# Kernel tuning notes

Hardware: AMD Instinct MI355X
Metric: run time of the kernel (lower is better)

The kernel has to match this reference:

```python
import jax, jax.numpy as jnp
import numpy as np

C = 256; HEADS = 8; LEVELS = 4; POINTS = 4; D = C // HEADS
SPATIAL = np.array([[96, 96], [48, 48], [24, 24], [12, 12]], dtype=np.int32)  # (H, W) per level
AREAS = SPATIAL[:, 0] * SPATIAL[:, 1]
HW = int(AREAS.sum())  # 12240
LSI = np.concatenate([[0], np.cumsum(AREAS)[:-1]]).astype(np.int32)
N = 1; Q = HW


def setup_inputs() -> dict:
    key = jax.random.key(0)
    ks = jax.random.split(key, 12)
    s = 0.02
    return {
        "query": jax.random.normal(ks[0], (N, Q, C), jnp.float32),
        "reference_points": jax.random.uniform(ks[1], (N, Q, LEVELS, 2), jnp.float32),
        "input_flatten": jax.random.normal(ks[2], (N, HW, C), jnp.float32),
        "input_spatial_shapes": jnp.asarray(SPATIAL),
        "input_level_start_index": jnp.asarray(LSI),
        "W_off": jax.random.normal(ks[3], (C, HEADS * LEVELS * POINTS * 2), jnp.float32) * s,
        "b_off": jax.random.normal(ks[4], (HEADS * LEVELS * POINTS * 2,), jnp.float32) * s,
        "W_attn": jax.random.normal(ks[5], (C, HEADS * LEVELS * POINTS), jnp.float32) * s,
        "b_attn": jax.random.normal(ks[6], (HEADS * LEVELS * POINTS,), jnp.float32) * s,
        "W_val": jax.random.normal(ks[7], (C, C), jnp.float32) * (1.0 / np.sqrt(C)),
        "b_val": jax.random.normal(ks[8], (C,), jnp.float32) * s,
        "W_out": jax.random.normal(ks[9], (C, C), jnp.float32) * (1.0 / np.sqrt(C)),
        "b_out": jax.random.normal(ks[10], (C,), jnp.float32) * s,
    }


def _ms_deform_attn(query, reference_points, input_flatten, sp, lsi,
                    W_off, b_off, W_attn, b_attn, W_val, b_val, W_out, b_out):
    n, q, c = query.shape
    hw = input_flatten.shape[1]
    # value projection -> [N, Hd, HW, D]
    value = (input_flatten @ W_val + b_val).reshape(n, hw, HEADS, D).transpose(0, 2, 1, 3)
    # sampling offsets [N,Q,Hd,L,P,2]
    off = (query @ W_off + b_off).reshape(n, q, HEADS, LEVELS, POINTS, 2)
    # attention weights softmaxed over L*P (done inside the fused CUDA kernel)
    attn = jax.nn.softmax((query @ W_attn + b_attn).reshape(n, q, HEADS, LEVELS * POINTS), axis=-1)
    attn = attn.reshape(n, q, HEADS, LEVELS, POINTS)
    # normalized sampling locations (reference_points last dim == 2 branch)
    norm = jnp.stack([sp[:, 1], sp[:, 0]], -1).astype(query.dtype)  # (W, H) per level
    loc = reference_points[:, :, None, :, None, :] + off / norm[None, None, None, :, None, :]
    Hl = sp[:, 0][None, None, None, :, None]
    Wl = sp[:, 1][None, None, None, :, None]
    start = lsi[None, None, None, :, None]
    # grid_sample-style (align_corners=False) pixel coordinates
    x = loc[..., 0] * Wl - 0.5
    y = loc[..., 1] * Hl - 0.5
    x0 = jnp.floor(x); y0 = jnp.floor(y)
    lx = x - x0; ly = y - y0
    x0i = x0.astype(jnp.int32); y0i = y0.astype(jnp.int32)

    def gather(yi, xi):
        valid = (xi >= 0) & (xi < Wl) & (yi >= 0) & (yi < Hl)
        idx = jnp.where(valid, start + yi * Wl + xi, 0)  # [N,Q,Hd,L,P]
        idx_t = idx.transpose(0, 2, 1, 3, 4).reshape(n, HEADS, q * LEVELS * POINTS, 1)
        g = jnp.take_along_axis(value, idx_t, axis=2)  # [N,Hd,Q*L*P,D]
        g = g.reshape(n, HEADS, q, LEVELS, POINTS, D)
        return g * valid.transpose(0, 2, 1, 3, 4)[..., None]

    def w(a):
        return a.transpose(0, 2, 1, 3, 4)[..., None]  # [N,Hd,Q,L,P,1]

    sampled = (gather(y0i, x0i) * w((1 - ly) * (1 - lx))
               + gather(y0i, x0i + 1) * w((1 - ly) * lx)
               + gather(y0i + 1, x0i) * w(ly * (1 - lx))
               + gather(y0i + 1, x0i + 1) * w(ly * lx))  # [N,Hd,Q,L,P,D]
    out = jnp.einsum('nhqlpd,nqhlp->nqhd', sampled, attn).reshape(n, q, c)
    return out @ W_out + b_out


def reference(query, reference_points, input_flatten, input_spatial_shapes, input_level_start_index,
              W_off, b_off, W_attn, b_attn, W_val, b_val, W_out, b_out):
    return _ms_deform_attn(query, reference_points, input_flatten,
                           input_spatial_shapes, input_level_start_index,
                           W_off, b_off, W_attn, b_attn, W_val, b_val, W_out, b_out)
```

## Files before the change

kernel.cpp:

```cpp
#include <hip/hip_runtime.h>

#define QTOT   12240
#define HWTOT  12240
#define KDIM   256

typedef float f32x4 __attribute__((ext_vector_type(4)));
typedef short s16x8 __attribute__((ext_vector_type(8)));
typedef unsigned short ushort_t;

__device__ __forceinline__ unsigned short f2b(float x) {
    union { float f; unsigned u; } c; c.f = x;
    unsigned r = c.u + 0x7fffu + ((c.u >> 16) & 1u);
    return (unsigned short)(r >> 16);
}

#define AEL 783360
__global__ __launch_bounds__(256) void conv_kernel(
    const float* __restrict__ inflat, const float* __restrict__ query,
    const float* __restrict__ W_val, const float* __restrict__ W_off,
    const float* __restrict__ W_attn, const float* __restrict__ W_out,
    const float* __restrict__ b_off, const float* __restrict__ b_attn,
    ushort_t* __restrict__ inflat_b, ushort_t* __restrict__ query_b,
    ushort_t* __restrict__ WvT, ushort_t* __restrict__ WcT,
    ushort_t* __restrict__ WoT, float* __restrict__ bcomb)
{
    int id = blockIdx.x * 256 + threadIdx.x;
    if (id < 2 * AEL) {
        const float* src = (id < AEL) ? inflat : query;
        ushort_t* dst = (id < AEL) ? inflat_b : query_b;
        int t = (id < AEL) ? id : id - AEL;
        float4 f = ((const float4*)src)[t];
        ushort4 o;
        o.x = f2b(f.x); o.y = f2b(f.y); o.z = f2b(f.z); o.w = f2b(f.w);
        ((ushort4*)dst)[t] = o;
    } else if (id < 2 * AEL + 65536) {
        int t = id - 2 * AEL;
        int n = t >> 8, k = t & 255;
        WvT[t] = f2b(W_val[k * 256 + n]);
    } else if (id < 2 * AEL + 65536 + 98304) {
        int t = id - (2 * AEL + 65536);
        int n = t >> 8, k = t & 255;
        float v = (n < 256) ? W_off[k * 256 + n] : W_attn[k * 128 + (n - 256)];
        WcT[t] = f2b(v);
    } else if (id < 2 * AEL + 65536 + 98304 + 65536) {
        int t = id - (2 * AEL + 65536 + 98304);
        int n = t >> 8, k = t & 255;
        WoT[t] = f2b(W_out[k * 256 + n]);
    } else if (id < 2 * AEL + 229376 + 384) {
        int t = id - (2 * AEL + 229376);
        bcomb[t] = (t < 256) ? b_off[t] : b_attn[t - 256];
    }
}

__device__ __forceinline__ void mm_core(
    const ushort_t* __restrict__ A, const ushort_t* __restrict__ BT,
    int bm, int bn, ushort_t As[64][72], ushort_t Bs[64][72], f32x4 acc[2][2])
{
    const int tid = threadIdx.x, lane = tid & 63, wave = tid >> 6;
    const int wr = wave >> 1, wc = wave & 1;
    const int r = tid >> 2, ks = (tid & 3) * 16;
    const bool aval = (bm + r) < QTOT;
    const int lr = lane & 15, g8 = (lane >> 4) * 8;

    for (int k0 = 0; k0 < KDIM; k0 += 64) {
        s16x8 a0 = (s16x8)0, a1 = (s16x8)0;
        if (aval) {
            const s16x8* s = (const s16x8*)(A + (size_t)(bm + r) * KDIM + k0 + ks);
            a0 = s[0]; a1 = s[1];
        }
        const s16x8* t = (const s16x8*)(BT + (size_t)(bn + r) * KDIM + k0 + ks);
        s16x8 b0 = t[0], b1 = t[1];
        if (k0) __syncthreads();
        *(s16x8*)&As[r][ks]     = a0;
        *(s16x8*)&As[r][ks + 8] = a1;
        *(s16x8*)&Bs[r][ks]     = b0;
        *(s16x8*)&Bs[r][ks + 8] = b1;
        __syncthreads();
#pragma unroll
        for (int kk = 0; kk < 2; ++kk) {
            s16x8 af[2], bf[2];
            af[0] = *(const s16x8*)&As[wr * 32 + lr][kk * 32 + g8];
            af[1] = *(const s16x8*)&As[wr * 32 + 16 + lr][kk * 32 + g8];
            bf[0] = *(const s16x8*)&Bs[wc * 32 + lr][kk * 32 + g8];
            bf[1] = *(const s16x8*)&Bs[wc * 32 + 16 + lr][kk * 32 + g8];
#pragma unroll
            for (int m = 0; m < 2; ++m)
#pragma unroll
                for (int n = 0; n < 2; ++n)
                    acc[m][n] = __builtin_amdgcn_mfma_f32_16x16x32_bf16(
                        af[m], bf[n], acc[m][n], 0, 0, 0);
        }
    }
}

__global__ __launch_bounds__(256) void gemm_vc(
    const ushort_t* __restrict__ Ab, const ushort_t* __restrict__ Qb,
    const ushort_t* __restrict__ WvT, const ushort_t* __restrict__ WcT,
    const float* __restrict__ b_val, const float* __restrict__ bcomb,
    ushort_t* __restrict__ projb, ushort_t* __restrict__ offb,
    float* __restrict__ logitf)
{
    __shared__ ushort_t As[64][72], Bs[64][72];
    const int b = blockIdx.x;
    const bool isval = b < 768;
    const ushort_t* A;
    const ushort_t* BT;
    const float* bias;
    int bm, bn;
    if (isval) { A = Ab; BT = WvT; bias = b_val;  bm = (b >> 2) * 64; bn = (b & 3) * 64; }
    else { int t = b - 768; A = Qb; BT = WcT; bias = bcomb; bm = (t / 6) * 64; bn = (t % 6) * 64; }

    f32x4 acc[2][2];
#pragma unroll
    for (int m = 0; m < 2; ++m)
#pragma unroll
        for (int n = 0; n < 2; ++n) acc[m][n] = (f32x4)0.f;

    mm_core(A, BT, bm, bn, As, Bs, acc);

    const int lane = threadIdx.x & 63, wave = threadIdx.x >> 6;
    const int wr = wave >> 1, wc = wave & 1;
    const int lr = lane & 15, rg = (lane >> 4) * 4;
#pragma unroll
    for (int n = 0; n < 2; ++n) {
        const int col = bn + wc * 32 + n * 16 + lr;
        const float bb = bias[col];
#pragma unroll
        for (int m = 0; m < 2; ++m)
#pragma unroll
            for (int rr = 0; rr < 4; ++rr) {
                const int row = bm + wr * 32 + m * 16 + rg + rr;
                if (row >= QTOT) continue;
                const float v = acc[m][n][rr] + bb;
                if (isval)            projb[(size_t)row * 256 + col] = f2b(v);
                else if (col < 256)   offb [(size_t)row * 256 + col] = f2b(v);
                else                  logitf[(size_t)row * 128 + col - 256] = v;
            }
    }
}

__global__ __launch_bounds__(256) void gemm_o(
    const ushort_t* __restrict__ Ab, const ushort_t* __restrict__ WoT,
    const float* __restrict__ b_out, float* __restrict__ out)
{
    __shared__ ushort_t As[64][72], Bs[64][72];
    const int b = blockIdx.x;
    const int bm = (b >> 2) * 64, bn = (b & 3) * 64;

    f32x4 acc[2][2];
#pragma unroll
    for (int m = 0; m < 2; ++m)
#pragma unroll
        for (int n = 0; n < 2; ++n) acc[m][n] = (f32x4)0.f;

    mm_core(Ab, WoT, bm, bn, As, Bs, acc);

    const int lane = threadIdx.x & 63, wave = threadIdx.x >> 6;
    const int wr = wave >> 1, wc = wave & 1;
    const int lr = lane & 15, rg = (lane >> 4) * 4;
#pragma unroll
    for (int n = 0; n < 2; ++n) {
        const int col = bn + wc * 32 + n * 16 + lr;
        const float bb = b_out[col];
#pragma unroll
        for (int m = 0; m < 2; ++m)
#pragma unroll
            for (int rr = 0; rr < 4; ++rr) {
                const int row = bm + wr * 32 + m * 16 + rg + rr;
                if (row < QTOT) out[(size_t)row * 256 + col] = acc[m][n][rr] + bb;
            }
    }
}

__global__ __launch_bounds__(256) void sample3(
    const float* __restrict__ rp, const ushort_t* __restrict__ offb,
    const float* __restrict__ logitf, const ushort_t* __restrict__ projb,
    const int* __restrict__ sp, const int* __restrict__ lsi,
    ushort_t* __restrict__ outpre)
{
    const int bid = blockIdx.x;
    const int q = (bid & 7) * (QTOT / 8) + (bid >> 3);
    const int tid = threadIdx.x;

    __shared__ int   s_idx[128][4];
    __shared__ float s_w[128][4];

    if (tid < 128) {
        const int l = (tid >> 2) & 3;
        float logit = logitf[(size_t)q * 128 + tid];
        float mx = logit;
#pragma unroll
        for (int d = 1; d < 16; d <<= 1) mx = fmaxf(mx, __shfl_xor(mx, d));
        float e = __expf(logit - mx);
        float s = e;
#pragma unroll
        for (int d = 1; d < 16; d <<= 1) s += __shfl_xor(s, d);
        const float aw = e / s;

        const unsigned opk = *(const unsigned*)&offb[(size_t)q * 256 + tid * 2];
        const float ox = __uint_as_float(opk << 16);
        const float oy = __uint_as_float(opk & 0xffff0000u);

        const int Hl = sp[l * 2], Wl = sp[l * 2 + 1], st = lsi[l];
        const float rx = rp[((size_t)q * 4 + l) * 2 + 0];
        const float ry = rp[((size_t)q * 4 + l) * 2 + 1];

        const float x = rx * (float)Wl + ox - 0.5f;
        const float y = ry * (float)Hl + oy - 0.5f;
        const float xf = floorf(x), yf = floorf(y);
        const int x0 = (int)xf, y0 = (int)yf;
        const float lx = x - xf, ly = y - yf;

        const bool vx0 = (x0 >= 0) && (x0 < Wl);
        const bool vx1 = (x0 + 1 >= 0) && (x0 + 1 < Wl);
        const bool vy0 = (y0 >= 0) && (y0 < Hl);
        const bool vy1 = (y0 + 1 >= 0) && (y0 + 1 < Hl);

        s_w[tid][0] = (vx0 && vy0) ? aw * (1.f - ly) * (1.f - lx) : 0.f;
        s_w[tid][1] = (vx1 && vy0) ? aw * (1.f - ly) * lx         : 0.f;
        s_w[tid][2] = (vx0 && vy1) ? aw * ly * (1.f - lx)         : 0.f;
        s_w[tid][3] = (vx1 && vy1) ? aw * ly * lx                 : 0.f;
        s_idx[tid][0] = (vx0 && vy0) ? st + y0 * Wl + x0           : 0;
        s_idx[tid][1] = (vx1 && vy0) ? st + y0 * Wl + x0 + 1       : 0;
        s_idx[tid][2] = (vx0 && vy1) ? st + (y0 + 1) * Wl + x0     : 0;
        s_idx[tid][3] = (vx1 && vy1) ? st + (y0 + 1) * Wl + x0 + 1 : 0;
    }
    __syncthreads();

    const int h = tid >> 5, qtr = (tid >> 3) & 3, c4 = tid & 7;
    const ushort_t* base = projb + h * 32 + c4 * 4;

    float a0 = 0.f, a1 = 0.f, a2 = 0.f, a3 = 0.f;
#pragma unroll
    for (int i = 0; i < 4; ++i) {
        const int slot = h * 16 + qtr * 4 + i;
        const int4   id4 = *(const int4*)s_idx[slot];
        const float4 w4  = *(const float4*)s_w[slot];
        uint2 v;
        v = *(const uint2*)(base + (size_t)id4.x * 256);
        a0 += w4.x * __uint_as_float(v.x << 16);
        a1 += w4.x * __uint_as_float(v.x & 0xffff0000u);
        a2 += w4.x * __uint_as_float(v.y << 16);
        a3 += w4.x * __uint_as_float(v.y & 0xffff0000u);
        v = *(const uint2*)(base + (size_t)id4.y * 256);
        a0 += w4.y * __uint_as_float(v.x << 16);
        a1 += w4.y * __uint_as_float(v.x & 0xffff0000u);
        a2 += w4.y * __uint_as_float(v.y << 16);
        a3 += w4.y * __uint_as_float(v.y & 0xffff0000u);
        v = *(const uint2*)(base + (size_t)id4.z * 256);
        a0 += w4.z * __uint_as_float(v.x << 16);
        a1 += w4.z * __uint_as_float(v.x & 0xffff0000u);
        a2 += w4.z * __uint_as_float(v.y << 16);
        a3 += w4.z * __uint_as_float(v.y & 0xffff0000u);
        v = *(const uint2*)(base + (size_t)id4.w * 256);
        a0 += w4.w * __uint_as_float(v.x << 16);
        a1 += w4.w * __uint_as_float(v.x & 0xffff0000u);
        a2 += w4.w * __uint_as_float(v.y << 16);
        a3 += w4.w * __uint_as_float(v.y & 0xffff0000u);
    }
    a0 += __shfl_xor(a0, 8);  a1 += __shfl_xor(a1, 8);
    a2 += __shfl_xor(a2, 8);  a3 += __shfl_xor(a3, 8);
    a0 += __shfl_xor(a0, 16); a1 += __shfl_xor(a1, 16);
    a2 += __shfl_xor(a2, 16); a3 += __shfl_xor(a3, 16);

    if ((tid & 24) == 0) {
        uint2 o;
        o.x = (unsigned)f2b(a0) | ((unsigned)f2b(a1) << 16);
        o.y = (unsigned)f2b(a2) | ((unsigned)f2b(a3) << 16);
        *(uint2*)&outpre[(size_t)q * 256 + h * 32 + c4 * 4] = o;
    }
}

extern "C" void kernel_launch(void* const* d_in, const int* in_sizes, int n_in,
                              void* d_out, int out_size, void* d_ws, size_t ws_size,
                              hipStream_t stream) {
    const float* query  = (const float*)d_in[0];
    const float* rp     = (const float*)d_in[1];
    const float* inflat = (const float*)d_in[2];
    const int*   sp     = (const int*)d_in[3];
    const int*   lsi    = (const int*)d_in[4];
    const float* W_off  = (const float*)d_in[5];
    const float* b_off  = (const float*)d_in[6];
    const float* W_attn = (const float*)d_in[7];
    const float* b_attn = (const float*)d_in[8];
    const float* W_val  = (const float*)d_in[9];
    const float* b_val  = (const float*)d_in[10];
    const float* W_out  = (const float*)d_in[11];
    const float* b_out  = (const float*)d_in[12];
    float* out = (float*)d_out;

    char* ws = (char*)d_ws;
    ushort_t* inflat_b = (ushort_t*)ws; ws += (size_t)HWTOT * 256 * 2;
    ushort_t* query_b  = (ushort_t*)ws; ws += (size_t)QTOT * 256 * 2;
    ushort_t* projb    = (ushort_t*)ws; ws += (size_t)HWTOT * 256 * 2;
    ushort_t* offb     = (ushort_t*)ws; ws += (size_t)QTOT * 256 * 2;
    float*    logitf   = (float*)ws;    ws += (size_t)QTOT * 128 * 4;
    ushort_t* outpre   = (ushort_t*)ws; ws += (size_t)QTOT * 256 * 2;
    ushort_t* WvT      = (ushort_t*)ws; ws += 65536 * 2;
    ushort_t* WcT      = (ushort_t*)ws; ws += 98304 * 2;
    ushort_t* WoT      = (ushort_t*)ws; ws += 65536 * 2;
    float*    bcomb    = (float*)ws;    ws += 384 * 4;

    dim3 blk(256);

    conv_kernel<<<dim3((2 * AEL + 229760 + 255) / 256), blk, 0, stream>>>(
        inflat, query, W_val, W_off, W_attn, W_out, b_off, b_attn,
        inflat_b, query_b, WvT, WcT, WoT, bcomb);

    gemm_vc<<<dim3(768 + 1152), blk, 0, stream>>>(
        inflat_b, query_b, WvT, WcT, b_val, bcomb, projb, offb, logitf);

    sample3<<<dim3(QTOT), blk, 0, stream>>>(rp, offb, logitf, projb, sp, lsi, outpre);

    gemm_o<<<dim3(768), blk, 0, stream>>>(outpre, WoT, b_out, out);
}
```

Measured before the change: 72.95 us.

## Fuse fp32-to-bf16 conversion into GEMMs, widen tiles, swizzle LDS, vectorize sampling

The separate activation conversion pass is removed. gemm1 now loads fp32 input/query rows directly, converts them to bf16 into a swizzled LDS A tile, and computes full-width output rows (32 rows × 256 or 384 cols) with B staged per k-slice. The sampling kernel processes two queries per block with 8-channel uint4 gathers and byte-offset indices. gemm_o uses 16-row tiles covering all 256 columns. This aims to cut global traffic and launch work, at the cost of more LDS per block and possibly lower occupancy.

Result: faster. 70.23 us (-3.7%).

```diff
diff --git a/kernel.cpp b/kernel.cpp
--- a/kernel.cpp
+++ b/kernel.cpp
@@ -1,8 +1,7 @@
 #include <hip/hip_runtime.h>
 
-#define QTOT   12240
-#define HWTOT  12240
-#define KDIM   256
+#define QTOT 12240
+#define KD   256
 
 typedef float f32x4 __attribute__((ext_vector_type(4)));
 typedef short s16x8 __attribute__((ext_vector_type(8)));
@@ -13,181 +12,173 @@
     unsigned r = c.u + 0x7fffu + ((c.u >> 16) & 1u);
     return (unsigned short)(r >> 16);
 }
-
-#define AEL 783360
-__global__ __launch_bounds__(256) void conv_kernel(
-    const float* __restrict__ inflat, const float* __restrict__ query,
+__device__ __forceinline__ int a_off(int row, int kb) { return row * 512 + (kb ^ ((row & 7) << 4)); }
+__device__ __forceinline__ int b_off(int n,   int kb) { return n * 128 + (kb ^ ((n & 7) << 4)); }
+
+__global__ __launch_bounds__(256) void prep(
     const float* __restrict__ W_val, const float* __restrict__ W_off,
     const float* __restrict__ W_attn, const float* __restrict__ W_out,
     const float* __restrict__ b_off, const float* __restrict__ b_attn,
-    ushort_t* __restrict__ inflat_b, ushort_t* __restrict__ query_b,
     ushort_t* __restrict__ WvT, ushort_t* __restrict__ WcT,
     ushort_t* __restrict__ WoT, float* __restrict__ bcomb)
 {
     int id = blockIdx.x * 256 + threadIdx.x;
-    if (id < 2 * AEL) {
-        const float* src = (id < AEL) ? inflat : query;
-        ushort_t* dst = (id < AEL) ? inflat_b : query_b;
-        int t = (id < AEL) ? id : id - AEL;
-        float4 f = ((const float4*)src)[t];
-        ushort4 o;
-        o.x = f2b(f.x); o.y = f2b(f.y); o.z = f2b(f.z); o.w = f2b(f.w);
-        ((ushort4*)dst)[t] = o;
-    } else if (id < 2 * AEL + 65536) {
-        int t = id - 2 * AEL;
-        int n = t >> 8, k = t & 255;
-        WvT[t] = f2b(W_val[k * 256 + n]);
-    } else if (id < 2 * AEL + 65536 + 98304) {
-        int t = id - (2 * AEL + 65536);
-        int n = t >> 8, k = t & 255;
+    if (id < 65536) { int n = id >> 8, k = id & 255; WvT[id] = f2b(W_val[k * 256 + n]); }
+    else if (id < 163840) {
+        int t = id - 65536; int n = t >> 8, k = t & 255;
         float v = (n < 256) ? W_off[k * 256 + n] : W_attn[k * 128 + (n - 256)];
         WcT[t] = f2b(v);
-    } else if (id < 2 * AEL + 65536 + 98304 + 65536) {
-        int t = id - (2 * AEL + 65536 + 98304);
-        int n = t >> 8, k = t & 255;
+    } else if (id < 229376) {
+        int t = id - 163840; int n = t >> 8, k = t & 255;
         WoT[t] = f2b(W_out[k * 256 + n]);
-    } else if (id < 2 * AEL + 229376 + 384) {
-        int t = id - (2 * AEL + 229376);
-        bcomb[t] = (t < 256) ? b_off[t] : b_attn[t - 256];
-    }
-}
-
-__device__ __forceinline__ void mm_core(
-    const ushort_t* __restrict__ A, const ushort_t* __restrict__ BT,
-    int bm, int bn, ushort_t As[64][72], ushort_t Bs[64][72], f32x4 acc[2][2])
-{
-    const int tid = threadIdx.x, lane = tid & 63, wave = tid >> 6;
-    const int wr = wave >> 1, wc = wave & 1;
-    const int r = tid >> 2, ks = (tid & 3) * 16;
-    const bool aval = (bm + r) < QTOT;
+    } else if (id < 229760) {
+        int t = id - 229376; bcomb[t] = (t < 256) ? b_off[t] : b_attn[t - 256];
+    }
+}
+
+template<int NF>
+__device__ __forceinline__ void stageB(const ushort_t* __restrict__ WT, int k0, char* Bs) {
+    const int tid = threadIdx.x;
+#pragma unroll
+    for (int e = 0; e < NF * 2; ++e) {
+        int u = e * 256 + tid;
+        int n = u >> 3, j = u & 7, js = j ^ (n & 7);
+        s16x8 v = *(const s16x8*)(WT + (size_t)n * KD + k0 + js * 8);
+        *(s16x8*)(Bs + n * 128 + j * 16) = v;
+    }
+}
+
+template<int NF>
+__device__ __forceinline__ void mm_full(const ushort_t* __restrict__ WT,
+                                        char* As, char* Bs, f32x4 (&acc)[2][NF])
+{
+    const int tid = threadIdx.x, lane = tid & 63, wc = tid >> 6;
     const int lr = lane & 15, g8 = (lane >> 4) * 8;
-
-    for (int k0 = 0; k0 < KDIM; k0 += 64) {
-        s16x8 a0 = (s16x8)0, a1 = (s16x8)0;
-        if (aval) {
-            const s16x8* s = (const s16x8*)(A + (size_t)(bm + r) * KDIM + k0 + ks);
-            a0 = s[0]; a1 = s[1];
-        }
-        const s16x8* t = (const s16x8*)(BT + (size_t)(bn + r) * KDIM + k0 + ks);
-        s16x8 b0 = t[0], b1 = t[1];
-        if (k0) __syncthreads();
-        *(s16x8*)&As[r][ks]     = a0;
-        *(s16x8*)&As[r][ks + 8] = a1;
-        *(s16x8*)&Bs[r][ks]     = b0;
-        *(s16x8*)&Bs[r][ks + 8] = b1;
+    for (int k0 = 0; k0 < KD; k0 += 64) {
         __syncthreads();
 #pragma unroll
         for (int kk = 0; kk < 2; ++kk) {
-            s16x8 af[2], bf[2];
-            af[0] = *(const s16x8*)&As[wr * 32 + lr][kk * 32 + g8];
-            af[1] = *(const s16x8*)&As[wr * 32 + 16 + lr][kk * 32 + g8];
-            bf[0] = *(const s16x8*)&Bs[wc * 32 + lr][kk * 32 + g8];
-            bf[1] = *(const s16x8*)&Bs[wc * 32 + 16 + lr][kk * 32 + g8];
-#pragma unroll
-            for (int m = 0; m < 2; ++m)
-#pragma unroll
-                for (int n = 0; n < 2; ++n)
-                    acc[m][n] = __builtin_amdgcn_mfma_f32_16x16x32_bf16(
-                        af[m], bf[n], acc[m][n], 0, 0, 0);
-        }
-    }
-}
-
-__global__ __launch_bounds__(256) void gemm_vc(
-    const ushort_t* __restrict__ Ab, const ushort_t* __restrict__ Qb,
+            const int kbB = (kk * 32 + g8) * 2;
+            const int kbA = (k0 + kk * 32 + g8) * 2;
+            s16x8 af0 = *(const s16x8*)(As + a_off(lr, kbA));
+            s16x8 af1 = *(const s16x8*)(As + a_off(16 + lr, kbA));
+#pragma unroll
+            for (int n = 0; n < NF; ++n) {
+                s16x8 bf = *(const s16x8*)(Bs + b_off(wc * NF * 16 + n * 16 + lr, kbB));
+                acc[0][n] = __builtin_amdgcn_mfma_f32_16x16x32_bf16(af0, bf, acc[0][n], 0, 0, 0);
+                acc[1][n] = __builtin_amdgcn_mfma_f32_16x16x32_bf16(af1, bf, acc[1][n], 0, 0, 0);
+            }
+        }
+        __syncthreads();
+        if (k0 < 192) stageB<NF>(WT, k0 + 64, Bs);
+    }
+}
+
+__global__ __launch_bounds__(256) void gemm1(
+    const float* __restrict__ inflat, const float* __restrict__ query,
     const ushort_t* __restrict__ WvT, const ushort_t* __restrict__ WcT,
     const float* __restrict__ b_val, const float* __restrict__ bcomb,
     ushort_t* __restrict__ projb, ushort_t* __restrict__ offb,
     float* __restrict__ logitf)
 {
-    __shared__ ushort_t As[64][72], Bs[64][72];
+    __shared__ char smem[16384 + 49152];
+    char* As = smem; char* Bs = smem + 16384;
     const int b = blockIdx.x;
-    const bool isval = b < 768;
-    const ushort_t* A;
-    const ushort_t* BT;
-    const float* bias;
-    int bm, bn;
-    if (isval) { A = Ab; BT = WvT; bias = b_val;  bm = (b >> 2) * 64; bn = (b & 3) * 64; }
-    else { int t = b - 768; A = Qb; BT = WcT; bias = bcomb; bm = (t / 6) * 64; bn = (t % 6) * 64; }
-
-    f32x4 acc[2][2];
-#pragma unroll
-    for (int m = 0; m < 2; ++m)
-#pragma unroll
-        for (int n = 0; n < 2; ++n) acc[m][n] = (f32x4)0.f;
-
-    mm_core(A, BT, bm, bn, As, Bs, acc);
-
-    const int lane = threadIdx.x & 63, wave = threadIdx.x >> 6;
-    const int wr = wave >> 1, wc = wave & 1;
+    const bool isval = b < 383;
+    const int bm = (isval ? b : b - 383) * 32;
+    const float* A = isval ? inflat : query;
+
+    {
+        const int row = threadIdx.x >> 3, c0 = (threadIdx.x & 7) * 32;
+        const int grow = bm + row;
+        float4 f[8];
+        if (grow < QTOT) {
+            const float4* s = (const float4*)(A + (size_t)grow * KD + c0);
+#pragma unroll
+            for (int i = 0; i < 8; ++i) f[i] = s[i];
+        } else {
+#pragma unroll
+            for (int i = 0; i < 8; ++i) f[i] = make_float4(0.f, 0.f, 0.f, 0.f);
+        }
+#pragma unroll
+        for (int i = 0; i < 4; ++i) {
+            s16x8 v;
+            v[0] = f2b(f[2*i].x);   v[1] = f2b(f[2*i].y);
+            v[2] = f2b(f[2*i].z);   v[3] = f2b(f[2*i].w);
+            v[4] = f2b(f[2*i+1].x); v[5] = f2b(f[2*i+1].y);
+            v[6] = f2b(f[2*i+1].z); v[7] = f2b(f[2*i+1].w);
+            *(s16x8*)(As + a_off(row, (c0 + i * 8) * 2)) = v;
+        }
+    }
+
+    const int lane = threadIdx.x & 63, wc = threadIdx.x >> 6;
     const int lr = lane & 15, rg = (lane >> 4) * 4;
-#pragma unroll
-    for (int n = 0; n < 2; ++n) {
-        const int col = bn + wc * 32 + n * 16 + lr;
-        const float bb = bias[col];
+
+    if (isval) {
+        f32x4 acc[2][4];
 #pragma unroll
         for (int m = 0; m < 2; ++m)
 #pragma unroll
-            for (int rr = 0; rr < 4; ++rr) {
-                const int row = bm + wr * 32 + m * 16 + rg + rr;
-                if (row >= QTOT) continue;
-                const float v = acc[m][n][rr] + bb;
-                if (isval)            projb[(size_t)row * 256 + col] = f2b(v);
-                else if (col < 256)   offb [(size_t)row * 256 + col] = f2b(v);
-                else                  logitf[(size_t)row * 128 + col - 256] = v;
-            }
-    }
-}
-
-__global__ __launch_bounds__(256) void gemm_o(
-    const ushort_t* __restrict__ Ab, const ushort_t* __restrict__ WoT,
-    const float* __restrict__ b_out, float* __restrict__ out)
-{
-    __shared__ ushort_t As[64][72], Bs[64][72];
-    const int b = blockIdx.x;
-    const int bm = (b >> 2) * 64, bn = (b & 3) * 64;
-
-    f32x4 acc[2][2];
-#pragma unroll
-    for (int m = 0; m < 2; ++m)
-#pragma unroll
-        for (int n = 0; n < 2; ++n) acc[m][n] = (f32x4)0.f;
-
-    mm_core(Ab, WoT, bm, bn, As, Bs, acc);
-
-    const int lane = threadIdx.x & 63, wave = threadIdx.x >> 6;
-    const int wr = wave >> 1, wc = wave & 1;
-    const int lr = lane & 15, rg = (lane >> 4) * 4;
-#pragma unroll
-    for (int n = 0; n < 2; ++n) {
-        const int col = bn + wc * 32 + n * 16 + lr;
-        const float bb = b_out[col];
+            for (int n = 0; n < 4; ++n) acc[m][n] = (f32x4)0.f;
+        stageB<4>(WvT, 0, Bs);
+        mm_full<4>(WvT, As, Bs, acc);
+#pragma unroll
+        for (int n = 0; n < 4; ++n) {
+            const int col = wc * 64 + n * 16 + lr;
+            const float bb = b_val[col];
+#pragma unroll
+            for (int m = 0; m < 2; ++m)
+#pragma unroll
+                for (int rr = 0; rr < 4; ++rr) {
+                    const int row = bm + m * 16 + rg + rr;
+                    if (row < QTOT) projb[(size_t)row * 256 + col] = f2b(acc[m][n][rr] + bb);
+                }
+        }
+    } else {
+        f32x4 acc[2][6];
 #pragma unroll
         for (int m = 0; m < 2; ++m)
 #pragma unroll
-            for (int rr = 0; rr < 4; ++rr) {
-                const int row = bm + wr * 32 + m * 16 + rg + rr;
-                if (row < QTOT) out[(size_t)row * 256 + col] = acc[m][n][rr] + bb;
-            }
-    }
-}
-
-__global__ __launch_bounds__(256) void sample3(
+            for (int n = 0; n < 6; ++n) acc[m][n] = (f32x4)0.f;
+        stageB<6>(WcT, 0, Bs);
+        mm_full<6>(WcT, As, Bs, acc);
+#pragma unroll
+        for (int n = 0; n < 6; ++n) {
+            const int col = wc * 96 + n * 16 + lr;
+            const float bb = bcomb[col];
+#pragma unroll
+            for (int m = 0; m < 2; ++m)
+#pragma unroll
+                for (int rr = 0; rr < 4; ++rr) {
+                    const int row = bm + m * 16 + rg + rr;
+                    if (row >= QTOT) continue;
+                    const float v = acc[m][n][rr] + bb;
+                    if (col < 256) offb[(size_t)row * 256 + col] = f2b(v);
+                    else           logitf[(size_t)row * 128 + col - 256] = v;
+                }
+        }
+    }
+}
+
+__global__ __launch_bounds__(256) void sample4(
     const float* __restrict__ rp, const ushort_t* __restrict__ offb,
     const float* __restrict__ logitf, const ushort_t* __restrict__ projb,
     const int* __restrict__ sp, const int* __restrict__ lsi,
     ushort_t* __restrict__ outpre)
 {
     const int bid = blockIdx.x;
-    const int q = (bid & 7) * (QTOT / 8) + (bid >> 3);
+    const int qpair = (bid & 7) * 765 + (bid >> 3);
     const int tid = threadIdx.x;
-
-    __shared__ int   s_idx[128][4];
-    __shared__ float s_w[128][4];
-
-    if (tid < 128) {
-        const int l = (tid >> 2) & 3;
-        float logit = logitf[(size_t)q * 128 + tid];
+    const int qi = tid >> 7;
+    const int q = qpair * 2 + qi;
+
+    __shared__ int   s_idx[256][4];
+    __shared__ float s_w[256][4];
+
+    {
+        const int t = tid & 127;
+        const int l = (t >> 2) & 3;
+        float logit = logitf[(size_t)q * 128 + t];
         float mx = logit;
 #pragma unroll
         for (int d = 1; d < 16; d <<= 1) mx = fmaxf(mx, __shfl_xor(mx, d));
@@ -197,7 +188,7 @@
         for (int d = 1; d < 16; d <<= 1) s += __shfl_xor(s, d);
         const float aw = e / s;
 
-        const unsigned opk = *(const unsigned*)&offb[(size_t)q * 256 + tid * 2];
+        const unsigned opk = *(const unsigned*)&offb[(size_t)q * 256 + t * 2];
         const float ox = __uint_as_float(opk << 16);
         const float oy = __uint_as_float(opk & 0xffff0000u);
 
@@ -220,54 +211,107 @@
         s_w[tid][1] = (vx1 && vy0) ? aw * (1.f - ly) * lx         : 0.f;
         s_w[tid][2] = (vx0 && vy1) ? aw * ly * (1.f - lx)         : 0.f;
         s_w[tid][3] = (vx1 && vy1) ? aw * ly * lx                 : 0.f;
-        s_idx[tid][0] = (vx0 && vy0) ? st + y0 * Wl + x0           : 0;
-        s_idx[tid][1] = (vx1 && vy0) ? st + y0 * Wl + x0 + 1       : 0;
-        s_idx[tid][2] = (vx0 && vy1) ? st + (y0 + 1) * Wl + x0     : 0;
-        s_idx[tid][3] = (vx1 && vy1) ? st + (y0 + 1) * Wl + x0 + 1 : 0;
+        s_idx[tid][0] = (vx0 && vy0) ? (st + y0 * Wl + x0) * 512           : 0;
+        s_idx[tid][1] = (vx1 && vy0) ? (st + y0 * Wl + x0 + 1) * 512       : 0;
+        s_idx[tid][2] = (vx0 && vy1) ? (st + (y0 + 1) * Wl + x0) * 512     : 0;
+        s_idx[tid][3] = (vx1 && vy1) ? (st + (y0 + 1) * Wl + x0 + 1) * 512 : 0;
     }
     __syncthreads();
 
-    const int h = tid >> 5, qtr = (tid >> 3) & 3, c4 = tid & 7;
-    const ushort_t* base = projb + h * 32 + c4 * 4;
-
-    float a0 = 0.f, a1 = 0.f, a2 = 0.f, a3 = 0.f;
-#pragma unroll
-    for (int i = 0; i < 4; ++i) {
-        const int slot = h * 16 + qtr * 4 + i;
+    const int tt = tid & 127;
+    const int h = tt >> 4, qtr = (tt >> 2) & 3, c8 = tt & 3;
+    const char* basec = (const char*)projb + (h * 32 + c8 * 8) * 2;
+
+    float a0 = 0, a1 = 0, a2 = 0, a3 = 0, a4 = 0, a5 = 0, a6 = 0, a7 = 0;
+#pragma unroll
+    for (int p = 0; p < 4; ++p) {
+        const int slot = qi * 128 + h * 16 + qtr * 4 + p;
         const int4   id4 = *(const int4*)s_idx[slot];
         const float4 w4  = *(const float4*)s_w[slot];
-        uint2 v;
-        v = *(const uint2*)(base + (size_t)id4.x * 256);
-        a0 += w4.x * __uint_as_float(v.x << 16);
-        a1 += w4.x * __uint_as_float(v.x & 0xffff0000u);
-        a2 += w4.x * __uint_as_float(v.y << 16);
-        a3 += w4.x * __uint_as_float(v.y & 0xffff0000u);
-        v = *(const uint2*)(base + (size_t)id4.y * 256);
-        a0 += w4.y * __uint_as_float(v.x << 16);
-        a1 += w4.y * __uint_as_float(v.x & 0xffff0000u);
-        a2 += w4.y * __uint_as_float(v.y << 16);
-        a3 += w4.y * __uint_as_float(v.y & 0xffff0000u);
-        v = *(const uint2*)(base + (size_t)id4.z * 256);
-        a0 += w4.z * __uint_as_float(v.x << 16);
-        a1 += w4.z * __uint_as_float(v.x & 0xffff0000u);
-        a2 += w4.z * __uint_as_float(v.y << 16);
-        a3 += w4.z * __uint_as_float(v.y & 0xffff0000u);
-        v = *(const uint2*)(base + (size_t)id4.w * 256);
-        a0 += w4.w * __uint_as_float(v.x << 16);
-        a1 += w4.w * __uint_as_float(v.x & 0xffff0000u);
-        a2 += w4.w * __uint_as_float(v.y << 16);
-        a3 += w4.w * __uint_as_float(v.y & 0xffff0000u);
-    }
-    a0 += __shfl_xor(a0, 8);  a1 += __shfl_xor(a1, 8);
-    a2 += __shfl_xor(a2, 8);  a3 += __shfl_xor(a3, 8);
-    a0 += __shfl_xor(a0, 16); a1 += __shfl_xor(a1, 16);
-    a2 += __shfl_xor(a2, 16); a3 += __shfl_xor(a3, 16);
-
-    if ((tid & 24) == 0) {
-        uint2 o;
+#pragma unroll
+        for (int c = 0; c < 4; ++c) {
+            const int   id = (c == 0) ? id4.x : (c == 1) ? id4.y : (c == 2) ? id4.z : id4.w;
+            const float w  = (c == 0) ? w4.x  : (c == 1) ? w4.y  : (c == 2) ? w4.z  : w4.w;
+            const uint4 v = *(const uint4*)(basec + id);
+            a0 += w * __uint_as_float(v.x << 16);
+            a1 += w * __uint_as_float(v.x & 0xffff0000u);
+            a2 += w * __uint_as_float(v.y << 16);
+            a3 += w * __uint_as_float(v.y & 0xffff0000u);
+            a4 += w * __uint_as_float(v.z << 16);
+            a5 += w * __uint_as_float(v.z & 0xffff0000u);
+            a6 += w * __uint_as_float(v.w << 16);
+            a7 += w * __uint_as_float(v.w & 0xffff0000u);
+        }
+    }
+    a0 += __shfl_xor(a0, 4); a1 += __shfl_xor(a1, 4);
+    a2 += __shfl_xor(a2, 4); a3 += __shfl_xor(a3, 4);
+    a4 += __shfl_xor(a4, 4); a5 += __shfl_xor(a5, 4);
+    a6 += __shfl_xor(a6, 4); a7 += __shfl_xor(a7, 4);
+    a0 += __shfl_xor(a0, 8); a1 += __shfl_xor(a1, 8);
+    a2 += __shfl_xor(a2, 8); a3 += __shfl_xor(a3, 8);
+    a4 += __shfl_xor(a4, 8); a5 += __shfl_xor(a5, 8);
+    a6 += __shfl_xor(a6, 8); a7 += __shfl_xor(a7, 8);
+
+    if (qtr == 0) {
+        uint4 o;
         o.x = (unsigned)f2b(a0) | ((unsigned)f2b(a1) << 16);
         o.y = (unsigned)f2b(a2) | ((unsigned)f2b(a3) << 16);
-        *(uint2*)&outpre[(size_t)q * 256 + h * 32 + c4 * 4] = o;
+        o.z = (unsigned)f2b(a4) | ((unsigned)f2b(a5) << 16);
+        o.w = (unsigned)f2b(a6) | ((unsigned)f2b(a7) << 16);
+        *(uint4*)&outpre[(size_t)q * 256 + h * 32 + c8 * 8] = o;
+    }
+}
+
+__global__ __launch_bounds__(256) void gemm_o(
+    const ushort_t* __restrict__ Ab, const ushort_t* __restrict__ WoT,
+    const float* __restrict__ b_out, float* __restrict__ out)
+{
+    __shared__ char smem[8192 + 32768];
+    char* As = smem; char* Bs = smem + 8192;
+    const int bm = blockIdx.x * 16;
+
+    {
+        const int row = threadIdx.x >> 4, cu = (threadIdx.x & 15) * 16;
+        const s16x8* s = (const s16x8*)(Ab + (size_t)(bm + row) * KD + cu);
+        s16x8 v0 = s[0], v1 = s[1];
+        *(s16x8*)(As + a_off(row, cu * 2))      = v0;
+        *(s16x8*)(As + a_off(row, cu * 2 + 16)) = v1;
+    }
+
+    f32x4 acc[4];
+#pragma unroll
+    for (int n = 0; n < 4; ++n) acc[n] = (f32x4)0.f;
+    stageB<4>(WoT, 0, Bs);
+
+    const int tid = threadIdx.x, lane = tid & 63, wc = tid >> 6;
+    const int lr = lane & 15, g8 = (lane >> 4) * 8;
+    for (int k0 = 0; k0 < KD; k0 += 64) {
+        __syncthreads();
+#pragma unroll
+        for (int kk = 0; kk < 2; ++kk) {
+            const int kbB = (kk * 32 + g8) * 2;
+            const int kbA = (k0 + kk * 32 + g8) * 2;
+            s16x8 af = *(const s16x8*)(As + a_off(lr, kbA));
+#pragma unroll
+            for (int n = 0; n < 4; ++n) {
+                s16x8 bf = *(const s16x8*)(Bs + b_off(wc * 64 + n * 16 + lr, kbB));
+                acc[n] = __builtin_amdgcn_mfma_f32_16x16x32_bf16(af, bf, acc[n], 0, 0, 0);
+            }
+        }
+        __syncthreads();
+        if (k0 < 192) stageB<4>(WoT, k0 + 64, Bs);
+    }
+
+    const int rg = (lane >> 4) * 4;
+#pragma unroll
+    for (int n = 0; n < 4; ++n) {
+        const int col = wc * 64 + n * 16 + lr;
+        const float bb = b_out[col];
+#pragma unroll
+        for (int rr = 0; rr < 4; ++rr) {
+            const int row = bm + rg + rr;
+            out[(size_t)row * 256 + col] = acc[n][rr] + bb;
+        }
     }
 }
 
@@ -290,27 +334,24 @@
     float* out = (float*)d_out;
 
     char* ws = (char*)d_ws;
-    ushort_t* inflat_b = (ushort_t*)ws; ws += (size_t)HWTOT * 256 * 2;
-    ushort_t* query_b  = (ushort_t*)ws; ws += (size_t)QTOT * 256 * 2;
-    ushort_t* projb    = (ushort_t*)ws; ws += (size_t)HWTOT * 256 * 2;
-    ushort_t* offb     = (ushort_t*)ws; ws += (size_t)QTOT * 256 * 2;
-    float*    logitf   = (float*)ws;    ws += (size_t)QTOT * 128 * 4;
-    ushort_t* outpre   = (ushort_t*)ws; ws += (size_t)QTOT * 256 * 2;
-    ushort_t* WvT      = (ushort_t*)ws; ws += 65536 * 2;
-    ushort_t* WcT      = (ushort_t*)ws; ws += 98304 * 2;
-    ushort_t* WoT      = (ushort_t*)ws; ws += 65536 * 2;
-    float*    bcomb    = (float*)ws;    ws += 384 * 4;
+    ushort_t* projb  = (ushort_t*)ws; ws += (size_t)QTOT * 256 * 2;
+    ushort_t* offb   = (ushort_t*)ws; ws += (size_t)QTOT * 256 * 2;
+    float*    logitf = (float*)ws;    ws += (size_t)QTOT * 128 * 4;
+    ushort_t* outpre = (ushort_t*)ws; ws += (size_t)QTOT * 256 * 2;
+    ushort_t* WvT    = (ushort_t*)ws; ws += 65536 * 2;
+    ushort_t* WcT    = (ushort_t*)ws; ws += 98304 * 2;
+    ushort_t* WoT    = (ushort_t*)ws; ws += 65536 * 2;
+    float*    bcomb  = (float*)ws;    ws += 384 * 4;
 
     dim3 blk(256);
 
-    conv_kernel<<<dim3((2 * AEL + 229760 + 255) / 256), blk, 0, stream>>>(
-        inflat, query, W_val, W_off, W_attn, W_out, b_off, b_attn,
-        inflat_b, query_b, WvT, WcT, WoT, bcomb);
-
-    gemm_vc<<<dim3(768 + 1152), blk, 0, stream>>>(
-        inflat_b, query_b, WvT, WcT, b_val, bcomb, projb, offb, logitf);
-
-    sample3<<<dim3(QTOT), blk, 0, stream>>>(rp, offb, logitf, projb, sp, lsi, outpre);
-
-    gemm_o<<<dim3(768), blk, 0, stream>>>(outpre, WoT, b_out, out);
-}
+    prep<<<dim3(898), blk, 0, stream>>>(W_val, W_off, W_attn, W_out, b_off, b_attn,
+                                        WvT, WcT, WoT, bcomb);
+
+    gemm1<<<dim3(766), blk, 0, stream>>>(inflat, query, WvT, WcT, b_val, bcomb,
+                                         projb, offb, logitf);
+
+    sample4<<<dim3(6120), blk, 0, stream>>>(rp, offb, logitf, projb, sp, lsi, outpre);
+
+    gemm_o<<<dim3(765), blk, 0, stream>>>(outpre, WoT, b_out, out);
+}
```
